# Kernel tuning notes

Measured on AMD Instinct MI355X. Metric: run time of the kernel, lower is better.

## Reference

```python
import jax, jax.numpy as jnp
import numpy as np

N = 1_000_000  # total nodes across the batch of graphs
B = 256        # number of graphs
D = 128        # embedding_dim


def setup_inputs() -> dict:
    key = jax.random.key(0)
    k1, k2, k3, k4, k5, k6, k7 = jax.random.split(key, 7)
    feat_i = jax.random.normal(k1, (N, D), dtype=jnp.float32)
    feat_u = jax.random.normal(k2, (B, D), dtype=jnp.float32)
    seg = jnp.sort(jax.random.randint(k3, (N,), 0, B, dtype=jnp.int32))
    s = 1.0 / np.sqrt(D)
    W_key = jax.random.normal(k4, (D, D), dtype=jnp.float32) * s
    W_user = jax.random.normal(k5, (D, D), dtype=jnp.float32) * s
    b_user = jax.random.normal(k6, (D,), dtype=jnp.float32) * s
    W_e = jax.random.normal(k7, (D, 1), dtype=jnp.float32) * s
    return {"feat_i": feat_i, "feat_u": feat_u, "seg": seg,
            "W_key": W_key, "W_user": W_user, "b_user": b_user, "W_e": W_e}


def reference(feat_i, feat_u, seg, W_key, W_user, b_user, W_e):
    num_graphs = feat_u.shape[0]
    # fc_key(feat_i): [N, d]
    key = feat_i @ W_key
    # fc_user(feat_u) broadcast to nodes (dgl.broadcast_nodes): [N, d]
    qry = (feat_u @ W_user + b_user)[seg]
    # fc_e(sigmoid(qry + key)): [N, 1]
    e = jax.nn.sigmoid(qry + key) @ W_e
    # segment_softmax over each graph's nodes (numerically stable)
    m = jax.ops.segment_max(e, seg, num_segments=num_graphs, indices_are_sorted=True)
    ex = jnp.exp(e - m[seg])
    denom = jax.ops.segment_sum(ex, seg, num_segments=num_graphs, indices_are_sorted=True)
    alpha = ex / denom[seg]  # [N, 1]
    # weighted segment sum of the (un-projected) item features
    rst = jax.ops.segment_sum(alpha * feat_i, seg, num_segments=num_graphs, indices_are_sorted=True)
    return rst  # [B, d]
```

## Files before the change

kernel.cpp:

```cpp
#include <hip/hip_runtime.h>
#include <hip/hip_bf16.h>
#include <stdint.h>

#define DIM 128
#define BSTRIDE 136

typedef float v4f __attribute__((ext_vector_type(4)));
typedef short v8s __attribute__((ext_vector_type(8)));

__device__ __forceinline__ unsigned short f2bf(float f) {
    union { float f; unsigned u; } c; c.f = f;
    unsigned r = c.u + 0x7fffu + ((c.u >> 16) & 1u);
    return (unsigned short)(r >> 16);
}

__global__ __launch_bounds__(256) void setup_kernel(const float* __restrict__ feat_u,
                                                    const float* __restrict__ W_user,
                                                    const float* __restrict__ b_user,
                                                    const float* __restrict__ W_key,
                                                    float* __restrict__ qry,
                                                    unsigned short* __restrict__ WkT,
                                                    float* __restrict__ numer,
                                                    float* __restrict__ denom,
                                                    int B) {
    __shared__ float fu[2][DIM];
    const int blk = blockIdx.x, t = threadIdx.x;
    const int qblocks = (B + 1) >> 1;
    if (blk < qblocks) {
        const int half = t >> 7, d = t & 127;
        const int b = blk * 2 + half;
        if (b < B) fu[half][d] = feat_u[b * DIM + d];
        __syncthreads();
        if (b < B) {
            float acc = b_user[d];
#pragma unroll 8
            for (int k = 0; k < DIM; ++k) acc += fu[half][k] * W_user[k * DIM + d];
            qry[b * DIM + d] = acc;
        }
    } else if (blk < qblocks + 64) {
        const int tid = (blk - qblocks) * 256 + t;
        const int k = tid >> 7, d = tid & 127;
        WkT[d * BSTRIDE + k] = f2bf(W_key[k * DIM + d]);
    } else {
        const int i = (blk - qblocks - 64) * 256 + t;
        if (i < B * DIM) numer[i] = 0.f;
        if (i < B) denom[i] = 0.f;
    }
}

__global__ __launch_bounds__(256) void fused_kernel(const float* __restrict__ feat_i,
                                                    const int* __restrict__ seg,
                                                    const unsigned short* __restrict__ WkT,
                                                    const float* __restrict__ qry,
                                                    const float* __restrict__ W_e,
                                                    float* __restrict__ numer,
                                                    float* __restrict__ denom,
                                                    int N) {
    __shared__ __align__(16) unsigned short Blds[DIM * BSTRIDE];
    __shared__ float We[DIM];
    int t = threadIdx.x;

    {
        const float4* src = (const float4*)WkT;
        float4* dst = (float4*)Blds;
        for (int i = t; i < (DIM * BSTRIDE) / 8; i += 256) dst[i] = src[i];
    }
    if (t < DIM) We[t] = W_e[t];
    __syncthreads();

    const int wave = t >> 6, lane = t & 63;
    const int m = lane & 15, quad = lane >> 4;
    const float2* f2 = (const float2*)feat_i;

    float2 wacc; wacc.x = 0.f; wacc.y = 0.f;
    float dsum = 0.f;
    int cur_sg = -1;

#define FLUSH()                                                            \
    do {                                                                   \
        atomicAdd(&numer[cur_sg * DIM + 2 * lane], wacc.x);                \
        atomicAdd(&numer[cur_sg * DIM + 2 * lane + 1], wacc.y);            \
        if (lane == 0) atomicAdd(&denom[cur_sg], dsum);                    \
        wacc.x = 0.f; wacc.y = 0.f; dsum = 0.f;                            \
    } while (0)

    for (int s = 0; s < 8; ++s) {
        const int strip = blockIdx.x * 512 + wave * 128 + s * 16;

        v8s a[4];
        const int n_a = strip + m;
        const bool va = (n_a < N);
        const float* arow = feat_i + (size_t)n_a * DIM + quad * 8;
#pragma unroll
        for (int kc = 0; kc < 4; ++kc) {
            float f[8];
            if (va) {
                float4 x0 = *(const float4*)(arow + kc * 32);
                float4 x1 = *(const float4*)(arow + kc * 32 + 4);
                f[0] = x0.x; f[1] = x0.y; f[2] = x0.z; f[3] = x0.w;
                f[4] = x1.x; f[5] = x1.y; f[6] = x1.z; f[7] = x1.w;
            } else {
#pragma unroll
                for (int j = 0; j < 8; ++j) f[j] = 0.f;
            }
            v8s af;
#pragma unroll
            for (int j = 0; j < 8; ++j) af[j] = (short)f2bf(f[j]);
            a[kc] = af;
        }

        v4f acc[8];
#pragma unroll
        for (int c = 0; c < 8; ++c) acc[c] = (v4f){0.f, 0.f, 0.f, 0.f};
#pragma unroll
        for (int c = 0; c < 8; ++c) {
            const unsigned short* brow = Blds + (c * 16 + m) * BSTRIDE + quad * 8;
#pragma unroll
            for (int kc = 0; kc < 4; ++kc) {
                v8s b = *(const v8s*)(brow + kc * 32);
                acc[c] = __builtin_amdgcn_mfma_f32_16x16x32_bf16(a[kc], b, acc[c], 0, 0, 0);
            }
        }

        float ev[4];
        int sgv[4];
#pragma unroll
        for (int r = 0; r < 4; ++r) {
            const int node = strip + quad * 4 + r;
            const bool nv = (node < N);
            const int sg = nv ? seg[node] : 0;
            sgv[r] = sg;
            const float* qrow = qry + sg * DIM;
            float partial = 0.f;
#pragma unroll
            for (int c = 0; c < 8; ++c) {
                const int d = c * 16 + m;
                const float x = acc[c][r] + qrow[d];
                const float sig = __builtin_amdgcn_rcpf(1.0f + __expf(-x));
                partial += sig * We[d];
            }
            partial += __shfl_xor(partial, 1);
            partial += __shfl_xor(partial, 2);
            partial += __shfl_xor(partial, 4);
            partial += __shfl_xor(partial, 8);
            ev[r] = __expf(partial);
        }

        if (strip < N) {
            const int sgf = __shfl(sgv[0], 0);
            const int sgl = __shfl(sgv[3], 48);
            if (sgf == sgl && strip + 15 < N) {
                if (sgf != cur_sg) {
                    if (cur_sg >= 0) FLUSH();
                    cur_sg = sgf;
                }
#pragma unroll
                for (int i = 0; i < 16; ++i) {
                    const float w = __shfl(ev[i & 3], (i >> 2) * 16);
                    const float2 v = f2[(size_t)(strip + i) * 64 + lane];
                    wacc.x += w * v.x;
                    wacc.y += w * v.y;
                    dsum += w;
                }
            } else {
#pragma unroll
                for (int i = 0; i < 16; ++i) {
                    const int n = strip + i;
                    if (n < N) {
                        const int sg = __shfl(sgv[i & 3], (i >> 2) * 16);
                        if (sg != cur_sg) {
                            if (cur_sg >= 0) FLUSH();
                            cur_sg = sg;
                        }
                        const float w = __shfl(ev[i & 3], (i >> 2) * 16);
                        const float2 v = f2[(size_t)n * 64 + lane];
                        wacc.x += w * v.x;
                        wacc.y += w * v.y;
                        dsum += w;
                    }
                }
            }
        }
    }

    if (cur_sg >= 0) FLUSH();
#undef FLUSH
}

__global__ void fin_kernel(const float* __restrict__ numer,
                           const float* __restrict__ denom,
                           float* __restrict__ out, int total) {
    int i = blockIdx.x * blockDim.x + threadIdx.x;
    if (i < total) {
        const float d = denom[i >> 7];
        out[i] = (d > 0.f) ? numer[i] / d : 0.f;
    }
}

extern "C" void kernel_launch(void* const* d_in, const int* in_sizes, int n_in,
                              void* d_out, int out_size, void* d_ws, size_t ws_size,
                              hipStream_t stream) {
    const float* feat_i = (const float*)d_in[0];
    const float* feat_u = (const float*)d_in[1];
    const int*   seg    = (const int*)d_in[2];
    const float* W_key  = (const float*)d_in[3];
    const float* W_user = (const float*)d_in[4];
    const float* b_user = (const float*)d_in[5];
    const float* W_e    = (const float*)d_in[6];
    float* out = (float*)d_out;

    const int N = in_sizes[2];
    const int B = in_sizes[1] / DIM;

    char* ws = (char*)d_ws;
    float*          qry   = (float*)ws;
    unsigned short* WkT   = (unsigned short*)(ws + 131072);
    float*          numer = (float*)(ws + 131072 + 34816);
    float*          denom = (float*)(ws + 131072 + 34816 + 131072);

    const int qblocks = (B + 1) >> 1;
    const int zblocks = (B * DIM + 255) / 256 + 1;
    setup_kernel<<<qblocks + 64 + zblocks, 256, 0, stream>>>(feat_u, W_user, b_user, W_key,
                                                             qry, WkT, numer, denom, B);

    const int nblk = (N + 511) / 512;
    fused_kernel<<<nblk, 256, 0, stream>>>(feat_i, seg, WkT, qry, W_e, numer, denom, N);

    fin_kernel<<<(B * DIM + 255) / 256, 256, 0, stream>>>(numer, denom, out, B * DIM);
}
```

Measured before the change: 849.7 us.

## Software-prefetch next strip of feat_i and hoist qry/W_e loads into registers

Double-buffers the A-operand rows of feat_i in registers, issuing the next strip's global loads before the current strip's MFMA and epilogue so memory latency overlaps with compute. The W_e values and, for single-segment strips, the qry row are loaded once into registers instead of per row. Launch bounds now request 3 blocks per SM, and the strip loop is fully unrolled. The trade-off is higher register pressure, which could cause spills under the occupancy hint.

```diff
diff --git a/kernel.cpp b/kernel.cpp
--- a/kernel.cpp
+++ b/kernel.cpp
@@ -48,14 +48,14 @@
     }
 }
 
-__global__ __launch_bounds__(256) void fused_kernel(const float* __restrict__ feat_i,
-                                                    const int* __restrict__ seg,
-                                                    const unsigned short* __restrict__ WkT,
-                                                    const float* __restrict__ qry,
-                                                    const float* __restrict__ W_e,
-                                                    float* __restrict__ numer,
-                                                    float* __restrict__ denom,
-                                                    int N) {
+__global__ __launch_bounds__(256, 3) void fused_kernel(const float* __restrict__ feat_i,
+                                                       const int* __restrict__ seg,
+                                                       const unsigned short* __restrict__ WkT,
+                                                       const float* __restrict__ qry,
+                                                       const float* __restrict__ W_e,
+                                                       float* __restrict__ numer,
+                                                       float* __restrict__ denom,
+                                                       int N) {
     __shared__ __align__(16) unsigned short Blds[DIM * BSTRIDE];
     __shared__ float We[DIM];
     int t = threadIdx.x;
@@ -70,7 +70,12 @@
 
     const int wave = t >> 6, lane = t & 63;
     const int m = lane & 15, quad = lane >> 4;
+    const int base = blockIdx.x * 512 + wave * 128;
     const float2* f2 = (const float2*)feat_i;
+
+    float we[8];
+#pragma unroll
+    for (int c = 0; c < 8; ++c) we[c] = We[c * 16 + m];
 
     float2 wacc; wacc.x = 0.f; wacc.y = 0.f;
     float dsum = 0.f;
@@ -84,29 +89,45 @@
         wacc.x = 0.f; wacc.y = 0.f; dsum = 0.f;                            \
     } while (0)
 
+    float4 pf[8];
+    {
+        const int n_a = base + m;
+        const float* arow = feat_i + (size_t)(n_a < N ? n_a : 0) * DIM + quad * 8;
+#pragma unroll
+        for (int kc = 0; kc < 4; ++kc) {
+            pf[2 * kc]     = *(const float4*)(arow + kc * 32);
+            pf[2 * kc + 1] = *(const float4*)(arow + kc * 32 + 4);
+        }
+    }
+
+#pragma unroll
     for (int s = 0; s < 8; ++s) {
-        const int strip = blockIdx.x * 512 + wave * 128 + s * 16;
+        const int strip = base + s * 16;
+        const bool va = (strip + m) < N;
 
         v8s a[4];
-        const int n_a = strip + m;
-        const bool va = (n_a < N);
-        const float* arow = feat_i + (size_t)n_a * DIM + quad * 8;
 #pragma unroll
         for (int kc = 0; kc < 4; ++kc) {
-            float f[8];
-            if (va) {
-                float4 x0 = *(const float4*)(arow + kc * 32);
-                float4 x1 = *(const float4*)(arow + kc * 32 + 4);
-                f[0] = x0.x; f[1] = x0.y; f[2] = x0.z; f[3] = x0.w;
-                f[4] = x1.x; f[5] = x1.y; f[6] = x1.z; f[7] = x1.w;
-            } else {
-#pragma unroll
-                for (int j = 0; j < 8; ++j) f[j] = 0.f;
-            }
             v8s af;
-#pragma unroll
-            for (int j = 0; j < 8; ++j) af[j] = (short)f2bf(f[j]);
+            af[0] = (short)f2bf(va ? pf[2 * kc].x : 0.f);
+            af[1] = (short)f2bf(va ? pf[2 * kc].y : 0.f);
+            af[2] = (short)f2bf(va ? pf[2 * kc].z : 0.f);
+            af[3] = (short)f2bf(va ? pf[2 * kc].w : 0.f);
+            af[4] = (short)f2bf(va ? pf[2 * kc + 1].x : 0.f);
+            af[5] = (short)f2bf(va ? pf[2 * kc + 1].y : 0.f);
+            af[6] = (short)f2bf(va ? pf[2 * kc + 1].z : 0.f);
+            af[7] = (short)f2bf(va ? pf[2 * kc + 1].w : 0.f);
             a[kc] = af;
+        }
+
+        if (s < 7) {
+            const int n_n = base + (s + 1) * 16 + m;
+            const float* arow = feat_i + (size_t)(n_n < N ? n_n : 0) * DIM + quad * 8;
+#pragma unroll
+            for (int kc = 0; kc < 4; ++kc) {
+                pf[2 * kc]     = *(const float4*)(arow + kc * 32);
+                pf[2 * kc + 1] = *(const float4*)(arow + kc * 32 + 4);
+            }
         }
 
         v4f acc[8];
@@ -127,29 +148,50 @@
 #pragma unroll
         for (int r = 0; r < 4; ++r) {
             const int node = strip + quad * 4 + r;
-            const bool nv = (node < N);
-            const int sg = nv ? seg[node] : 0;
-            sgv[r] = sg;
-            const float* qrow = qry + sg * DIM;
-            float partial = 0.f;
-#pragma unroll
-            for (int c = 0; c < 8; ++c) {
-                const int d = c * 16 + m;
-                const float x = acc[c][r] + qrow[d];
-                const float sig = __builtin_amdgcn_rcpf(1.0f + __expf(-x));
-                partial += sig * We[d];
-            }
-            partial += __shfl_xor(partial, 1);
-            partial += __shfl_xor(partial, 2);
-            partial += __shfl_xor(partial, 4);
-            partial += __shfl_xor(partial, 8);
-            ev[r] = __expf(partial);
+            sgv[r] = (node < N) ? seg[node] : 0;
+        }
+        const int sgf = __shfl(sgv[0], 0);
+        const int sgl = __shfl(sgv[3], 48);
+        const bool uni = (sgf == sgl) && (strip + 15 < N);
+
+        if (uni) {
+            float q[8];
+#pragma unroll
+            for (int c = 0; c < 8; ++c) q[c] = qry[sgf * DIM + c * 16 + m];
+#pragma unroll
+            for (int r = 0; r < 4; ++r) {
+                float partial = 0.f;
+#pragma unroll
+                for (int c = 0; c < 8; ++c) {
+                    const float x = acc[c][r] + q[c];
+                    partial += __builtin_amdgcn_rcpf(1.0f + __expf(-x)) * we[c];
+                }
+                partial += __shfl_xor(partial, 1);
+                partial += __shfl_xor(partial, 2);
+                partial += __shfl_xor(partial, 4);
+                partial += __shfl_xor(partial, 8);
+                ev[r] = __expf(partial);
+            }
+        } else {
+#pragma unroll
+            for (int r = 0; r < 4; ++r) {
+                const float* qrow = qry + sgv[r] * DIM;
+                float partial = 0.f;
+#pragma unroll
+                for (int c = 0; c < 8; ++c) {
+                    const float x = acc[c][r] + qrow[c * 16 + m];
+                    partial += __builtin_amdgcn_rcpf(1.0f + __expf(-x)) * we[c];
+                }
+                partial += __shfl_xor(partial, 1);
+                partial += __shfl_xor(partial, 2);
+                partial += __shfl_xor(partial, 4);
+                partial += __shfl_xor(partial, 8);
+                ev[r] = __expf(partial);
+            }
         }
 
         if (strip < N) {
-            const int sgf = __shfl(sgv[0], 0);
-            const int sgl = __shfl(sgv[3], 48);
-            if (sgf == sgl && strip + 15 < N) {
+            if (uni) {
                 if (sgf != cur_sg) {
                     if (cur_sg >= 0) FLUSH();
                     cur_sg = sgf;
```

Measured after the change: 872.8 us. +2.7%, slower.
